# Optimization experiments

Hardware: AMD Instinct MI355X
Metric: run time of the kernel (lower is better)

The kernel has to match this reference:

```python
import jax, jax.numpy as jnp
import numpy as np

K = 8
DIM = 64
NUM_BLOCKS = 12
BN_EPS = 1e-5
LRELU_SLOPE = 0.01  # torch nn.LeakyReLU default negative_slope


def knn_indices(xyz, k):
    # xyz: [b, 3, n] -> idx [b, n, k] of k nearest neighbors (self included)
    x = jnp.transpose(xyz, (0, 2, 1))  # [b, n, 3]
    sq = jnp.sum(x * x, axis=-1)  # [b, n]
    d2 = sq[:, :, None] - 2.0 * jnp.einsum('bnd,bmd->bnm', x, x) + sq[:, None, :]
    _, idx = jax.lax.top_k(-d2, k)  # k smallest distances
    return idx


def group_point(points, idx):
    # points [b, d, n], idx [b, n, k] -> grouped [b, d, k, n]
    g = jax.vmap(lambda p, i: p[:, i])(points, idx)  # [b, d, n, k]
    return jnp.transpose(g, (0, 1, 3, 2))


def setup_inputs() -> dict:
    key = jax.random.key(0)
    ks = jax.random.split(key, 6)
    b, n = 8, 4096
    xyz = jax.random.normal(ks[0], (b, 3, n), dtype=jnp.float32)
    points = jax.random.normal(ks[1], (b, DIM, n), dtype=jnp.float32)
    # per-block params (note: the module's second Conv2d per block is never used
    # in forward — layers[4*idx+2] is applied to both center and grouped points)
    conv_w = jax.random.normal(ks[2], (NUM_BLOCKS, DIM, DIM), dtype=jnp.float32) * (1.0 / np.sqrt(DIM))
    conv_b = jax.random.normal(ks[3], (NUM_BLOCKS, DIM), dtype=jnp.float32) * 0.01
    bn_gamma = 1.0 + 0.1 * jax.random.normal(ks[4], (NUM_BLOCKS, DIM), dtype=jnp.float32)
    bn_beta = 0.1 * jax.random.normal(ks[5], (NUM_BLOCKS, DIM), dtype=jnp.float32)
    return {"xyz": xyz, "points": points, "conv_w": conv_w, "conv_b": conv_b,
            "bn_gamma": bn_gamma, "bn_beta": bn_beta}


def reference(xyz, points, conv_w, conv_b, bn_gamma, bn_beta):
    idx = knn_indices(xyz, K)  # fixed graph, computed once in block 0

    def block(p, params):
        w, b, g, be = params  # [DIM,DIM], [DIM], [DIM], [DIM]
        shortcut = p
        # BatchNorm1d (training-mode batch stats over batch & point dims)
        mean = jnp.mean(p, axis=(0, 2), keepdims=True)
        var = jnp.var(p, axis=(0, 2), keepdims=True)
        h = (p - mean) * jax.lax.rsqrt(var + BN_EPS) * g[None, :, None] + be[None, :, None]
        # LeakyReLU
        h = jnp.where(h >= 0, h, LRELU_SLOPE * h)
        # gather neighbor features: [b, d, k, n]
        grouped = group_point(h, idx)
        # shared 1x1 conv on center and grouped points
        center = jnp.einsum('od,bdn->bon', w, h) + b[None, :, None]            # [b,d,n]
        gconv = jnp.einsum('od,bdkn->bokn', w, grouped) + b[None, :, None, None]  # [b,d,k,n]
        # mean over concat([center[:, :, None], gconv], axis=2) == (center + sum_k gconv) / (k+1)
        new_p = (center + jnp.sum(gconv, axis=2)) / (K + 1) + shortcut
        return new_p, None

    out, _ = jax.lax.scan(block, points, (conv_w, conv_b, bn_gamma, bn_beta))
    return out
```

## Files before the change

kernel.cpp:

```cpp
#include <hip/hip_runtime.h>
#include <hip/hip_bf16.h>

#define NB     8
#define NPTS   4096
#define DIMC   64
#define KNN_K  8
#define NBLK   12
#define NREP   8

__global__ void zero_stats_kernel(float* __restrict__ stats) {
    int i = threadIdx.x + blockIdx.x * 256;
    if (i < 13 * NREP * 128) stats[i] = 0.0f;
}

__global__ __launch_bounds__(256) void prep_kernel(
        const float* __restrict__ xyz, float4* __restrict__ pts4g) {
#pragma clang fp contract(off)
    int g = blockIdx.x * 256 + threadIdx.x;
    int b = g >> 12, j = g & 4095;
    const float* xb = xyz + (size_t)b * 3 * NPTS;
    float x = xb[j];
    float y = xb[NPTS + j];
    float z = xb[2 * NPTS + j];
    float sq = (x * x + y * y) + z * z;
    pts4g[g] = make_float4(x, y, z, sq);
}

__global__ __launch_bounds__(256) void cast_kernel(
        const float* __restrict__ pts,
        float* __restrict__ P0, float* __restrict__ stats0) {
    __shared__ __align__(16) float tr[64 * 65];
    __shared__ float slotA[4 * 64], slotB[4 * 64];
    int wg = blockIdx.x;
    int b = wg & 7;
    int n0 = (wg >> 3) << 6;
    int rep = (wg >> 3) & (NREP - 1);
    int tid = threadIdx.x;
    int lane6 = tid & 63;
    int grp = tid >> 6;

    #pragma unroll
    for (int k = 0; k < 16; ++k) {
        int d = grp + (k << 2);
        float v = pts[(((size_t)((b << 6) + d)) << 12) + n0 + lane6];
        tr[d * 65 + lane6] = v;
    }
    __syncthreads();
    int c = lane6;
    float s = 0.0f, s2 = 0.0f;
    #pragma unroll
    for (int k = 0; k < 16; ++k) {
        int p = grp + (k << 2);
        float v = tr[c * 65 + p];
        P0[((size_t)((b << 12) + n0 + p)) * 64 + c] = v;
        s += v; s2 += v * v;
    }
    slotA[grp * 64 + c] = s;
    slotB[grp * 64 + c] = s2;
    __syncthreads();
    if (tid < 64) {
        float t = slotA[tid] + slotA[64 + tid] + slotA[128 + tid] + slotA[192 + tid];
        atomicAdd(&stats0[rep * 128 + tid], t);
    } else if (tid < 128) {
        int cc = tid - 64;
        float t = slotB[cc] + slotB[64 + cc] + slotB[128 + cc] + slotB[192 + cc];
        atomicAdd(&stats0[rep * 128 + 64 + cc], t);
    }
}

__global__ __launch_bounds__(512) void knn_kernel(
        const float4* __restrict__ pts4g, int* __restrict__ idx) {
#pragma clang fp contract(off)
    __shared__ __align__(16) float4 cand[2048];
    __shared__ double stash[4 * 9 * 128];
    int wg = blockIdx.x;
    int b = wg >> 5;
    int q0 = (wg & 31) << 7;
    int tid = threadIdx.x;

    int lane  = tid & 63;
    int wave  = tid >> 6;
    int chunk = wave & 3;
    int qgrp  = wave >> 2;
    int q_l   = (qgrp << 6) | lane;

    const float4* cb = pts4g + ((size_t)b << 12);
    float4 qp = cb[q0 + q_l];

    double k0, k1, k2, k3, k4, k5, k6, k7;
    k0 = k1 = k2 = k3 = k4 = k5 = k6 = k7 = __builtin_inf();
    float bd7f = 3.4e38f;

    for (int half = 0; half < 2; ++half) {
        if (half) __syncthreads();
        #pragma unroll
        for (int k = 0; k < 4; ++k)
            cand[tid + (k << 9)] = cb[(half << 11) + tid + (k << 9)];
        __syncthreads();

        int jl0 = chunk << 9;
        int jg0 = (half << 11) | (chunk << 9);
        int jstart = 0;

        if (half == 0) {
            for (int jo = 0; jo < 128; jo += 8) {
                float d2v[8];
                #pragma unroll
                for (int u = 0; u < 8; ++u) {
                    float4 p = cand[jl0 + jo + u];
                    float dot = (qp.x * p.x + qp.y * p.y) + qp.z * p.z;
                    d2v[u] = (qp.w - 2.0f * dot) + p.w;
                }
                #pragma unroll
                for (int u = 0; u < 8; ++u) {
                    unsigned long long kb =
                        __double_as_longlong((double)d2v[u]) |
                        (unsigned long long)(jg0 + jo + u);
                    double key = __longlong_as_double(kb);
                    double n0 = fmin(k0, key);
                    double n1 = fmin(k1, fmax(k0, key));
                    double n2 = fmin(k2, fmax(k1, key));
                    double n3 = fmin(k3, fmax(k2, key));
                    double n4 = fmin(k4, fmax(k3, key));
                    double n5 = fmin(k5, fmax(k4, key));
                    double n6 = fmin(k6, fmax(k5, key));
                    double n7 = fmin(k7, fmax(k6, key));
                    k0 = n0; k1 = n1; k2 = n2; k3 = n3;
                    k4 = n4; k5 = n5; k6 = n6; k7 = n7;
                }
            }
            bd7f = (float)k7;
            jstart = 128;
        }

        for (int jo = jstart; jo < 512; jo += 8) {
            float d2v[8];
            unsigned hm = 0u;
            #pragma unroll
            for (int u = 0; u < 8; ++u) {
                float4 p = cand[jl0 + jo + u];
                float dot = (qp.x * p.x + qp.y * p.y) + qp.z * p.z;
                float d2 = (qp.w - 2.0f * dot) + p.w;
                d2v[u] = d2;
                hm |= (d2 < bd7f) ? (1u << u) : 0u;
            }
            while (__any(hm != 0u)) {
                if (hm) {
                    int u = __builtin_ctz(hm);
                    hm &= hm - 1u;
                    float t0 = (u & 1) ? d2v[1] : d2v[0];
                    float t1 = (u & 1) ? d2v[3] : d2v[2];
                    float t2 = (u & 1) ? d2v[5] : d2v[4];
                    float t3 = (u & 1) ? d2v[7] : d2v[6];
                    float s0 = (u & 2) ? t1 : t0;
                    float s1 = (u & 2) ? t3 : t2;
                    float d2 = (u & 4) ? s1 : s0;
                    unsigned long long kb =
                        __double_as_longlong((double)d2) |
                        (unsigned long long)(jg0 + jo + u);
                    double key = __longlong_as_double(kb);
                    double n0 = fmin(k0, key);
                    double n1 = fmin(k1, fmax(k0, key));
                    double n2 = fmin(k2, fmax(k1, key));
                    double n3 = fmin(k3, fmax(k2, key));
                    double n4 = fmin(k4, fmax(k3, key));
                    double n5 = fmin(k5, fmax(k4, key));
                    double n6 = fmin(k6, fmax(k5, key));
                    double n7 = fmin(k7, fmax(k6, key));
                    k0 = n0; k1 = n1; k2 = n2; k3 = n3;
                    k4 = n4; k5 = n5; k6 = n6; k7 = n7;
                }
            }
            bd7f = (float)k7;
        }
    }

    {
        double* S = &stash[(chunk * 9) * 128 + q_l];
        S[0 * 128] = k0; S[1 * 128] = k1; S[2 * 128] = k2; S[3 * 128] = k3;
        S[4 * 128] = k4; S[5 * 128] = k5; S[6 * 128] = k6; S[7 * 128] = k7;
        S[8 * 128] = __builtin_inf();
    }
    __syncthreads();

    if (tid < 128) {
        int h0 = 0, h1 = 0, h2 = 0, h3 = 0;
        int* op = idx + ((size_t)(b * NPTS + q0 + tid)) * 8;
        #pragma unroll
        for (int t = 0; t < 8; ++t) {
            double b0 = stash[(0 * 9 + h0) * 128 + tid];
            double b1 = stash[(1 * 9 + h1) * 128 + tid];
            double b2 = stash[(2 * 9 + h2) * 128 + tid];
            double b3 = stash[(3 * 9 + h3) * 128 + tid];
            double best = b0; int bc = 0;
            if (b1 < best) { best = b1; bc = 1; }
            if (b2 < best) { best = b2; bc = 2; }
            if (b3 < best) { best = b3; bc = 3; }
            h0 += (bc == 0); h1 += (bc == 1);
            h2 += (bc == 2); h3 += (bc == 3);
            op[t] = (int)(__double_as_longlong(best) & 0xFFFULL);
        }
    }
}

__global__ __launch_bounds__(256) void block_kernel(
        const float* __restrict__ Pin, float* __restrict__ Pout,
        const float* __restrict__ statsIn, float* __restrict__ statsOut,
        const float* __restrict__ Wp, const float* __restrict__ Bp,
        const float* __restrict__ Gp, const float* __restrict__ Betap,
        const int* __restrict__ gidx, float* __restrict__ dout, int last) {
    __shared__ __align__(16) float Wt[64 * 68];
    __shared__ __align__(16) float mt[64 * 68];
    __shared__ __align__(16) float selft[64 * 64];
    __shared__ __align__(16) int   idxl[64 * 8];
    __shared__ __align__(16) float scale_l[64], shift_l[64], bias_l[64];
    __shared__ float slot[4 * 128];

    int wg = blockIdx.x;
    int b = wg & 7;
    int n0 = (wg >> 3) << 6;
    int rep = (wg >> 3) & (NREP - 1);
    int tid = threadIdx.x;

    const float* Pb = Pin + (((size_t)b) << 18);

    if (tid < 128) {
        ((int4*)idxl)[tid] = ((const int4*)(gidx + ((size_t)(b * NPTS + n0)) * 8))[tid];
    }
    #pragma unroll
    for (int k = 0; k < 4; ++k) {
        int lin = tid + (k << 8);
        ((float4*)selft)[lin] = ((const float4*)&Pb[(size_t)n0 << 6])[lin];
    }
    #pragma unroll
    for (int k = 0; k < 16; ++k) {
        int lin = tid + (k << 8);
        int o = lin >> 6, d = lin & 63;
        Wt[d * 68 + o] = Wp[lin];
    }
    if (tid < 64) {
        int c = tid;
        float sum = 0.0f, sumsq = 0.0f;
        #pragma unroll
        for (int r = 0; r < NREP; ++r) {
            sum   += statsIn[r * 128 + c];
            sumsq += statsIn[r * 128 + 64 + c];
        }
        float mean = sum * (1.0f / 32768.0f);
        float var  = sumsq * (1.0f / 32768.0f) - mean * mean;
        float rs   = 1.0f / sqrtf(var + 1e-5f);
        float sc   = Gp[c] * rs;
        scale_l[c] = sc;
        shift_l[c] = Betap[c] - mean * sc;
        bias_l[c]  = Bp[c];
    }
    __syncthreads();

    {
        int cq = tid & 15;
        int pg = tid >> 4;
        int c4 = cq << 2;
        float4 sc4 = *(const float4*)&scale_l[c4];
        float4 sh4 = *(const float4*)&shift_l[c4];
        #pragma unroll
        for (int i = 0; i < 4; ++i) {
            int pt = (pg << 2) + i;
            int4 ja = *(const int4*)&idxl[pt * 8];
            int4 jb = *(const int4*)&idxl[pt * 8 + 4];
            float4 v[9];
            v[0] = *(const float4*)&selft[(pt << 6) + c4];
            v[1] = *(const float4*)&Pb[(((size_t)ja.x) << 6) + c4];
            v[2] = *(const float4*)&Pb[(((size_t)ja.y) << 6) + c4];
            v[3] = *(const float4*)&Pb[(((size_t)ja.z) << 6) + c4];
            v[4] = *(const float4*)&Pb[(((size_t)ja.w) << 6) + c4];
            v[5] = *(const float4*)&Pb[(((size_t)jb.x) << 6) + c4];
            v[6] = *(const float4*)&Pb[(((size_t)jb.y) << 6) + c4];
            v[7] = *(const float4*)&Pb[(((size_t)jb.z) << 6) + c4];
            v[8] = *(const float4*)&Pb[(((size_t)jb.w) << 6) + c4];
            float4 a = make_float4(0.f, 0.f, 0.f, 0.f);
            #pragma unroll
            for (int k = 0; k < 9; ++k) {
                float hx = v[k].x * sc4.x + sh4.x;
                float hy = v[k].y * sc4.y + sh4.y;
                float hz = v[k].z * sc4.z + sh4.z;
                float hw = v[k].w * sc4.w + sh4.w;
                a.x += fmaxf(hx, 0.01f * hx);
                a.y += fmaxf(hy, 0.01f * hy);
                a.z += fmaxf(hz, 0.01f * hz);
                a.w += fmaxf(hw, 0.01f * hw);
            }
            mt[(c4 + 0) * 68 + pt] = a.x * (1.0f / 9.0f);
            mt[(c4 + 1) * 68 + pt] = a.y * (1.0f / 9.0f);
            mt[(c4 + 2) * 68 + pt] = a.z * (1.0f / 9.0f);
            mt[(c4 + 3) * 68 + pt] = a.w * (1.0f / 9.0f);
        }
    }
    __syncthreads();

    int o0 = (tid & 15) << 2;
    int p0 = (tid >> 4) << 2;
    float4 acc[4];
    {
        float4 bias4 = *(const float4*)&bias_l[o0];
        acc[0] = bias4; acc[1] = bias4; acc[2] = bias4; acc[3] = bias4;
    }
    #pragma unroll
    for (int d = 0; d < 64; ++d) {
        float4 wv = *(const float4*)&Wt[d * 68 + o0];
        float4 a  = *(const float4*)&mt[d * 68 + p0];
        acc[0].x += wv.x * a.x; acc[0].y += wv.y * a.x; acc[0].z += wv.z * a.x; acc[0].w += wv.w * a.x;
        acc[1].x += wv.x * a.y; acc[1].y += wv.y * a.y; acc[1].z += wv.z * a.y; acc[1].w += wv.w * a.y;
        acc[2].x += wv.x * a.z; acc[2].y += wv.y * a.z; acc[2].z += wv.z * a.z; acc[2].w += wv.w * a.z;
        acc[3].x += wv.x * a.w; acc[3].y += wv.y * a.w; acc[3].z += wv.z * a.w; acc[3].w += wv.w * a.w;
    }

    #pragma unroll
    for (int j = 0; j < 4; ++j) {
        float4 r = *(const float4*)&selft[((p0 + j) << 6) + o0];
        acc[j].x += r.x; acc[j].y += r.y; acc[j].z += r.z; acc[j].w += r.w;
    }

    if (!last) {
        float* PbOut = Pout + ((((size_t)b) << 12) + n0) * 64;
        #pragma unroll
        for (int j = 0; j < 4; ++j)
            *(float4*)&PbOut[((size_t)(p0 + j)) * 64 + o0] = acc[j];

        float4 s, s2;
        s.x = acc[0].x + acc[1].x + acc[2].x + acc[3].x;
        s.y = acc[0].y + acc[1].y + acc[2].y + acc[3].y;
        s.z = acc[0].z + acc[1].z + acc[2].z + acc[3].z;
        s.w = acc[0].w + acc[1].w + acc[2].w + acc[3].w;
        s2.x = acc[0].x*acc[0].x + acc[1].x*acc[1].x + acc[2].x*acc[2].x + acc[3].x*acc[3].x;
        s2.y = acc[0].y*acc[0].y + acc[1].y*acc[1].y + acc[2].y*acc[2].y + acc[3].y*acc[3].y;
        s2.z = acc[0].z*acc[0].z + acc[1].z*acc[1].z + acc[2].z*acc[2].z + acc[3].z*acc[3].z;
        s2.w = acc[0].w*acc[0].w + acc[1].w*acc[1].w + acc[2].w*acc[2].w + acc[3].w*acc[3].w;
        #pragma unroll
        for (int m = 16; m <= 32; m <<= 1) {
            s.x += __shfl_xor(s.x, m, 64);  s.y += __shfl_xor(s.y, m, 64);
            s.z += __shfl_xor(s.z, m, 64);  s.w += __shfl_xor(s.w, m, 64);
            s2.x += __shfl_xor(s2.x, m, 64); s2.y += __shfl_xor(s2.y, m, 64);
            s2.z += __shfl_xor(s2.z, m, 64); s2.w += __shfl_xor(s2.w, m, 64);
        }
        if ((tid & 63) < 16) {
            int w = tid >> 6;
            slot[w * 128 + o0 + 0] = s.x;  slot[w * 128 + o0 + 1] = s.y;
            slot[w * 128 + o0 + 2] = s.z;  slot[w * 128 + o0 + 3] = s.w;
            slot[w * 128 + 64 + o0 + 0] = s2.x; slot[w * 128 + 64 + o0 + 1] = s2.y;
            slot[w * 128 + 64 + o0 + 2] = s2.z; slot[w * 128 + 64 + o0 + 3] = s2.w;
        }
        __syncthreads();
        if (tid < 128) {
            float t = slot[tid] + slot[128 + tid] + slot[256 + tid] + slot[384 + tid];
            atomicAdd(&statsOut[rep * 128 + tid], t);
        }
    } else {
        __syncthreads();
        float* stage = mt;
        #pragma unroll
        for (int j = 0; j < 4; ++j) {
            stage[(o0 + 0) * 64 + p0 + j] = acc[j].x;
            stage[(o0 + 1) * 64 + p0 + j] = acc[j].y;
            stage[(o0 + 2) * 64 + p0 + j] = acc[j].z;
            stage[(o0 + 3) * 64 + p0 + j] = acc[j].w;
        }
        __syncthreads();
        #pragma unroll
        for (int k = 0; k < 16; ++k) {
            int lin = tid + (k << 8);
            int o = lin >> 6, pt = lin & 63;
            dout[(((size_t)((b << 6) + o)) << 12) + n0 + pt] = stage[lin];
        }
    }
}

extern "C" void kernel_launch(void* const* d_in, const int* in_sizes, int n_in,
                              void* d_out, int out_size, void* d_ws, size_t ws_size,
                              hipStream_t stream) {
    const float* xyz    = (const float*)d_in[0];
    const float* pts    = (const float*)d_in[1];
    const float* conv_w = (const float*)d_in[2];
    const float* conv_b = (const float*)d_in[3];
    const float* gamma  = (const float*)d_in[4];
    const float* beta   = (const float*)d_in[5];
    float* out = (float*)d_out;

    char* ws = (char*)d_ws;
    float*  P0    = (float*)(ws);
    float*  P1    = (float*)(ws + (size_t)8 * 1024 * 1024);
    int*    idx   = (int*)  (ws + (size_t)16 * 1024 * 1024);
    float*  stats = (float*)(ws + (size_t)17 * 1024 * 1024);
    float4* pts4g = (float4*)(ws + (size_t)18 * 1024 * 1024);

    zero_stats_kernel<<<52, 256, 0, stream>>>(stats);
    prep_kernel<<<128, 256, 0, stream>>>(xyz, pts4g);
    cast_kernel<<<512, 256, 0, stream>>>(pts, P0, stats);
    knn_kernel<<<256, 512, 0, stream>>>(pts4g, idx);

    float* Pbuf[2] = {P0, P1};
    for (int t = 0; t < NBLK; ++t) {
        block_kernel<<<512, 256, 0, stream>>>(
            Pbuf[t & 1], Pbuf[(t + 1) & 1],
            stats + (size_t)t * NREP * 128, stats + (size_t)(t + 1) * NREP * 128,
            conv_w + (size_t)t * 4096, conv_b + (size_t)t * 64,
            gamma + (size_t)t * 64, beta + (size_t)t * 64,
            idx, out, (t == NBLK - 1) ? 1 : 0);
    }
}
```

Measured before the change: 310.1 us.

## Split KNN candidate scan across 8 waves per 64 queries, double grid

Each workgroup of the KNN kernel now handles 64 queries instead of 128, with all 8 waves working on the same queries, each scanning a 256-candidate chunk per half. The final merge combines 8 sorted partial lists instead of 4, and the grid doubles to 512 workgroups with batch-interleaved mapping. This aims to raise parallelism and occupancy for the KNN search across the GPU's compute units. The cost is twice as many candidate loads into shared memory per query, a shorter warm-up before threshold pruning starts, and a longer merge step.

```diff
diff --git a/kernel.cpp b/kernel.cpp
--- a/kernel.cpp
+++ b/kernel.cpp
@@ -72,20 +72,17 @@
         const float4* __restrict__ pts4g, int* __restrict__ idx) {
 #pragma clang fp contract(off)
     __shared__ __align__(16) float4 cand[2048];
-    __shared__ double stash[4 * 9 * 128];
+    __shared__ double stash[8 * 9 * 64];
     int wg = blockIdx.x;
-    int b = wg >> 5;
-    int q0 = (wg & 31) << 7;
+    int b = wg & 7;
+    int q0 = (wg >> 3) << 6;
     int tid = threadIdx.x;
 
     int lane  = tid & 63;
-    int wave  = tid >> 6;
-    int chunk = wave & 3;
-    int qgrp  = wave >> 2;
-    int q_l   = (qgrp << 6) | lane;
+    int chunk = tid >> 6;
 
     const float4* cb = pts4g + ((size_t)b << 12);
-    float4 qp = cb[q0 + q_l];
+    float4 qp = cb[q0 + lane];
 
     double k0, k1, k2, k3, k4, k5, k6, k7;
     k0 = k1 = k2 = k3 = k4 = k5 = k6 = k7 = __builtin_inf();
@@ -98,12 +95,12 @@
             cand[tid + (k << 9)] = cb[(half << 11) + tid + (k << 9)];
         __syncthreads();
 
-        int jl0 = chunk << 9;
-        int jg0 = (half << 11) | (chunk << 9);
+        int jl0 = chunk << 8;
+        int jg0 = (half << 11) | (chunk << 8);
         int jstart = 0;
 
         if (half == 0) {
-            for (int jo = 0; jo < 128; jo += 8) {
+            for (int jo = 0; jo < 32; jo += 8) {
                 float d2v[8];
                 #pragma unroll
                 for (int u = 0; u < 8; ++u) {
@@ -130,10 +127,10 @@
                 }
             }
             bd7f = (float)k7;
-            jstart = 128;
-        }
-
-        for (int jo = jstart; jo < 512; jo += 8) {
+            jstart = 32;
+        }
+
+        for (int jo = jstart; jo < 256; jo += 8) {
             float d2v[8];
             unsigned hm = 0u;
             #pragma unroll
@@ -176,28 +173,38 @@
     }
 
     {
-        double* S = &stash[(chunk * 9) * 128 + q_l];
-        S[0 * 128] = k0; S[1 * 128] = k1; S[2 * 128] = k2; S[3 * 128] = k3;
-        S[4 * 128] = k4; S[5 * 128] = k5; S[6 * 128] = k6; S[7 * 128] = k7;
-        S[8 * 128] = __builtin_inf();
+        double* S = &stash[(chunk * 9) * 64 + lane];
+        S[0 * 64] = k0; S[1 * 64] = k1; S[2 * 64] = k2; S[3 * 64] = k3;
+        S[4 * 64] = k4; S[5 * 64] = k5; S[6 * 64] = k6; S[7 * 64] = k7;
+        S[8 * 64] = __builtin_inf();
     }
     __syncthreads();
 
-    if (tid < 128) {
-        int h0 = 0, h1 = 0, h2 = 0, h3 = 0;
+    if (tid < 64) {
+        int h0 = 0, h1 = 0, h2 = 0, h3 = 0, h4 = 0, h5 = 0, h6 = 0, h7 = 0;
         int* op = idx + ((size_t)(b * NPTS + q0 + tid)) * 8;
         #pragma unroll
         for (int t = 0; t < 8; ++t) {
-            double b0 = stash[(0 * 9 + h0) * 128 + tid];
-            double b1 = stash[(1 * 9 + h1) * 128 + tid];
-            double b2 = stash[(2 * 9 + h2) * 128 + tid];
-            double b3 = stash[(3 * 9 + h3) * 128 + tid];
-            double best = b0; int bc = 0;
-            if (b1 < best) { best = b1; bc = 1; }
-            if (b2 < best) { best = b2; bc = 2; }
-            if (b3 < best) { best = b3; bc = 3; }
+            double c0 = stash[(0 * 9 + h0) * 64 + tid];
+            double c1 = stash[(1 * 9 + h1) * 64 + tid];
+            double c2 = stash[(2 * 9 + h2) * 64 + tid];
+            double c3 = stash[(3 * 9 + h3) * 64 + tid];
+            double c4 = stash[(4 * 9 + h4) * 64 + tid];
+            double c5 = stash[(5 * 9 + h5) * 64 + tid];
+            double c6 = stash[(6 * 9 + h6) * 64 + tid];
+            double c7 = stash[(7 * 9 + h7) * 64 + tid];
+            double best = c0; int bc = 0;
+            if (c1 < best) { best = c1; bc = 1; }
+            if (c2 < best) { best = c2; bc = 2; }
+            if (c3 < best) { best = c3; bc = 3; }
+            if (c4 < best) { best = c4; bc = 4; }
+            if (c5 < best) { best = c5; bc = 5; }
+            if (c6 < best) { best = c6; bc = 6; }
+            if (c7 < best) { best = c7; bc = 7; }
             h0 += (bc == 0); h1 += (bc == 1);
             h2 += (bc == 2); h3 += (bc == 3);
+            h4 += (bc == 4); h5 += (bc == 5);
+            h6 += (bc == 6); h7 += (bc == 7);
             op[t] = (int)(__double_as_longlong(best) & 0xFFFULL);
         }
     }
@@ -395,7 +402,7 @@
     zero_stats_kernel<<<52, 256, 0, stream>>>(stats);
     prep_kernel<<<128, 256, 0, stream>>>(xyz, pts4g);
     cast_kernel<<<512, 256, 0, stream>>>(pts, P0, stats);
-    knn_kernel<<<256, 512, 0, stream>>>(pts4g, idx);
+    knn_kernel<<<512, 512, 0, stream>>>(pts4g, idx);
 
     float* Pbuf[2] = {P0, P1};
     for (int t = 0; t < NBLK; ++t) {
```

Measured after the change: 313.2 us. Within noise of the previous version (+1.0%).

## Fuse twelve block launches into one persistent kernel with grid barriers

Applied to the files above, without the earlier changes.

The twelve per-block launches are replaced by a single persistent kernel that loops over blocks and uses an atomic-counter grid barrier between them, removing per-launch overhead and idle gaps. The stats zeroing is folded into the prep kernel, which also clears the barrier counters. The kNN kernel drops its LDS candidate staging and instead streams candidates directly from global memory with register double-buffering, each wave scanning a 1024-point chunk. The grid barrier assumes all 512 workgroups are co-resident, otherwise it deadlocks. Each block also reloads the weights and its tile every iteration.

```diff
diff --git a/kernel.cpp b/kernel.cpp
--- a/kernel.cpp
+++ b/kernel.cpp
@@ -7,16 +7,15 @@
 #define KNN_K  8
 #define NBLK   12
 #define NREP   8
-
-__global__ void zero_stats_kernel(float* __restrict__ stats) {
-    int i = threadIdx.x + blockIdx.x * 256;
-    if (i < 13 * NREP * 128) stats[i] = 0.0f;
-}
+#define NWG    512
 
 __global__ __launch_bounds__(256) void prep_kernel(
-        const float* __restrict__ xyz, float4* __restrict__ pts4g) {
+        const float* __restrict__ xyz, float4* __restrict__ pts4g,
+        float* __restrict__ stats, int* __restrict__ bar) {
 #pragma clang fp contract(off)
     int g = blockIdx.x * 256 + threadIdx.x;
+    if (g < 13 * NREP * 128) stats[g] = 0.0f;
+    if (g < 16) bar[g] = 0;
     int b = g >> 12, j = g & 4095;
     const float* xb = xyz + (size_t)b * 3 * NPTS;
     float x = xb[j];
@@ -68,10 +67,22 @@
     }
 }
 
+#define INS(KEY) do { \
+    double key = (KEY); \
+    double n0 = fmin(k0, key); \
+    double n1 = fmin(k1, fmax(k0, key)); \
+    double n2 = fmin(k2, fmax(k1, key)); \
+    double n3 = fmin(k3, fmax(k2, key)); \
+    double n4 = fmin(k4, fmax(k3, key)); \
+    double n5 = fmin(k5, fmax(k4, key)); \
+    double n6 = fmin(k6, fmax(k5, key)); \
+    double n7 = fmin(k7, fmax(k6, key)); \
+    k0 = n0; k1 = n1; k2 = n2; k3 = n3; \
+    k4 = n4; k5 = n5; k6 = n6; k7 = n7; } while (0)
+
 __global__ __launch_bounds__(512) void knn_kernel(
         const float4* __restrict__ pts4g, int* __restrict__ idx) {
 #pragma clang fp contract(off)
-    __shared__ __align__(16) float4 cand[2048];
     __shared__ double stash[4 * 9 * 128];
     int wg = blockIdx.x;
     int b = wg >> 5;
@@ -91,87 +102,72 @@
     k0 = k1 = k2 = k3 = k4 = k5 = k6 = k7 = __builtin_inf();
     float bd7f = 3.4e38f;
 
-    for (int half = 0; half < 2; ++half) {
-        if (half) __syncthreads();
-        #pragma unroll
-        for (int k = 0; k < 4; ++k)
-            cand[tid + (k << 9)] = cb[(half << 11) + tid + (k << 9)];
-        __syncthreads();
-
-        int jl0 = chunk << 9;
-        int jg0 = (half << 11) | (chunk << 9);
-        int jstart = 0;
-
-        if (half == 0) {
-            for (int jo = 0; jo < 128; jo += 8) {
-                float d2v[8];
-                #pragma unroll
-                for (int u = 0; u < 8; ++u) {
-                    float4 p = cand[jl0 + jo + u];
-                    float dot = (qp.x * p.x + qp.y * p.y) + qp.z * p.z;
-                    d2v[u] = (qp.w - 2.0f * dot) + p.w;
-                }
-                #pragma unroll
-                for (int u = 0; u < 8; ++u) {
-                    unsigned long long kb =
-                        __double_as_longlong((double)d2v[u]) |
-                        (unsigned long long)(jg0 + jo + u);
-                    double key = __longlong_as_double(kb);
-                    double n0 = fmin(k0, key);
-                    double n1 = fmin(k1, fmax(k0, key));
-                    double n2 = fmin(k2, fmax(k1, key));
-                    double n3 = fmin(k3, fmax(k2, key));
-                    double n4 = fmin(k4, fmax(k3, key));
-                    double n5 = fmin(k5, fmax(k4, key));
-                    double n6 = fmin(k6, fmax(k5, key));
-                    double n7 = fmin(k7, fmax(k6, key));
-                    k0 = n0; k1 = n1; k2 = n2; k3 = n3;
-                    k4 = n4; k5 = n5; k6 = n6; k7 = n7;
-                }
-            }
-            bd7f = (float)k7;
-            jstart = 128;
-        }
-
-        for (int jo = jstart; jo < 512; jo += 8) {
-            float d2v[8];
-            unsigned hm = 0u;
-            #pragma unroll
-            for (int u = 0; u < 8; ++u) {
-                float4 p = cand[jl0 + jo + u];
-                float dot = (qp.x * p.x + qp.y * p.y) + qp.z * p.z;
-                float d2 = (qp.w - 2.0f * dot) + p.w;
-                d2v[u] = d2;
-                hm |= (d2 < bd7f) ? (1u << u) : 0u;
-            }
-            while (__any(hm != 0u)) {
-                if (hm) {
-                    int u = __builtin_ctz(hm);
-                    hm &= hm - 1u;
-                    float t0 = (u & 1) ? d2v[1] : d2v[0];
-                    float t1 = (u & 1) ? d2v[3] : d2v[2];
-                    float t2 = (u & 1) ? d2v[5] : d2v[4];
-                    float t3 = (u & 1) ? d2v[7] : d2v[6];
-                    float s0 = (u & 2) ? t1 : t0;
-                    float s1 = (u & 2) ? t3 : t2;
-                    float d2 = (u & 4) ? s1 : s0;
-                    unsigned long long kb =
-                        __double_as_longlong((double)d2) |
-                        (unsigned long long)(jg0 + jo + u);
-                    double key = __longlong_as_double(kb);
-                    double n0 = fmin(k0, key);
-                    double n1 = fmin(k1, fmax(k0, key));
-                    double n2 = fmin(k2, fmax(k1, key));
-                    double n3 = fmin(k3, fmax(k2, key));
-                    double n4 = fmin(k4, fmax(k3, key));
-                    double n5 = fmin(k5, fmax(k4, key));
-                    double n6 = fmin(k6, fmax(k5, key));
-                    double n7 = fmin(k7, fmax(k6, key));
-                    k0 = n0; k1 = n1; k2 = n2; k3 = n3;
-                    k4 = n4; k5 = n5; k6 = n6; k7 = n7;
-                }
-            }
-            bd7f = (float)k7;
+    int chu = __builtin_amdgcn_readfirstlane(chunk);
+    const float4* cc = cb + ((size_t)chu << 10);
+    int jg0 = chu << 10;
+
+    float4 pc[8];
+    #pragma unroll
+    for (int u = 0; u < 8; ++u) pc[u] = cc[u];
+
+    for (int jo = 0; jo < 128; jo += 8) {
+        float4 pn[8];
+        #pragma unroll
+        for (int u = 0; u < 8; ++u) pn[u] = cc[jo + 8 + u];
+        float d2v[8];
+        #pragma unroll
+        for (int u = 0; u < 8; ++u) {
+            float dot = (qp.x * pc[u].x + qp.y * pc[u].y) + qp.z * pc[u].z;
+            d2v[u] = (qp.w - 2.0f * dot) + pc[u].w;
+        }
+        #pragma unroll
+        for (int u = 0; u < 8; ++u) {
+            unsigned long long kb =
+                __double_as_longlong((double)d2v[u]) |
+                (unsigned long long)(jg0 + jo + u);
+            INS(__longlong_as_double(kb));
+        }
+        #pragma unroll
+        for (int u = 0; u < 8; ++u) pc[u] = pn[u];
+    }
+    bd7f = (float)k7;
+
+    for (int jo = 128; jo < 1024; jo += 8) {
+        float4 pn[8];
+        if (jo + 8 < 1024) {
+            #pragma unroll
+            for (int u = 0; u < 8; ++u) pn[u] = cc[jo + 8 + u];
+        }
+        float d2v[8];
+        unsigned hm = 0u;
+        #pragma unroll
+        for (int u = 0; u < 8; ++u) {
+            float dot = (qp.x * pc[u].x + qp.y * pc[u].y) + qp.z * pc[u].z;
+            float d2 = (qp.w - 2.0f * dot) + pc[u].w;
+            d2v[u] = d2;
+            hm |= (d2 < bd7f) ? (1u << u) : 0u;
+        }
+        while (__any(hm != 0u)) {
+            if (hm) {
+                int u = __builtin_ctz(hm);
+                hm &= hm - 1u;
+                float t0 = (u & 1) ? d2v[1] : d2v[0];
+                float t1 = (u & 1) ? d2v[3] : d2v[2];
+                float t2 = (u & 1) ? d2v[5] : d2v[4];
+                float t3 = (u & 1) ? d2v[7] : d2v[6];
+                float s0 = (u & 2) ? t1 : t0;
+                float s1 = (u & 2) ? t3 : t2;
+                float d2 = (u & 4) ? s1 : s0;
+                unsigned long long kb =
+                    __double_as_longlong((double)d2) |
+                    (unsigned long long)(jg0 + jo + u);
+                INS(__longlong_as_double(kb));
+            }
+        }
+        bd7f = (float)k7;
+        if (jo + 8 < 1024) {
+            #pragma unroll
+            for (int u = 0; u < 8; ++u) pc[u] = pn[u];
         }
     }
 
@@ -203,12 +199,13 @@
     }
 }
 
-__global__ __launch_bounds__(256) void block_kernel(
-        const float* __restrict__ Pin, float* __restrict__ Pout,
-        const float* __restrict__ statsIn, float* __restrict__ statsOut,
-        const float* __restrict__ Wp, const float* __restrict__ Bp,
-        const float* __restrict__ Gp, const float* __restrict__ Betap,
-        const int* __restrict__ gidx, float* __restrict__ dout, int last) {
+__global__ __launch_bounds__(256) void blocks_kernel(
+        float* __restrict__ P0, float* __restrict__ P1,
+        float* __restrict__ stats,
+        const float* __restrict__ conv_w, const float* __restrict__ conv_b,
+        const float* __restrict__ gamma, const float* __restrict__ beta,
+        const int* __restrict__ gidx, float* __restrict__ dout,
+        int* __restrict__ bar) {
     __shared__ __align__(16) float Wt[64 * 68];
     __shared__ __align__(16) float mt[64 * 68];
     __shared__ __align__(16) float selft[64 * 64];
@@ -222,154 +219,181 @@
     int rep = (wg >> 3) & (NREP - 1);
     int tid = threadIdx.x;
 
-    const float* Pb = Pin + (((size_t)b) << 18);
-
     if (tid < 128) {
         ((int4*)idxl)[tid] = ((const int4*)(gidx + ((size_t)(b * NPTS + n0)) * 8))[tid];
     }
-    #pragma unroll
-    for (int k = 0; k < 4; ++k) {
-        int lin = tid + (k << 8);
-        ((float4*)selft)[lin] = ((const float4*)&Pb[(size_t)n0 << 6])[lin];
-    }
-    #pragma unroll
-    for (int k = 0; k < 16; ++k) {
-        int lin = tid + (k << 8);
-        int o = lin >> 6, d = lin & 63;
-        Wt[d * 68 + o] = Wp[lin];
-    }
-    if (tid < 64) {
-        int c = tid;
-        float sum = 0.0f, sumsq = 0.0f;
-        #pragma unroll
-        for (int r = 0; r < NREP; ++r) {
-            sum   += statsIn[r * 128 + c];
-            sumsq += statsIn[r * 128 + 64 + c];
-        }
-        float mean = sum * (1.0f / 32768.0f);
-        float var  = sumsq * (1.0f / 32768.0f) - mean * mean;
-        float rs   = 1.0f / sqrtf(var + 1e-5f);
-        float sc   = Gp[c] * rs;
-        scale_l[c] = sc;
-        shift_l[c] = Betap[c] - mean * sc;
-        bias_l[c]  = Bp[c];
-    }
-    __syncthreads();
-
-    {
-        int cq = tid & 15;
-        int pg = tid >> 4;
-        int c4 = cq << 2;
-        float4 sc4 = *(const float4*)&scale_l[c4];
-        float4 sh4 = *(const float4*)&shift_l[c4];
-        #pragma unroll
-        for (int i = 0; i < 4; ++i) {
-            int pt = (pg << 2) + i;
-            int4 ja = *(const int4*)&idxl[pt * 8];
-            int4 jb = *(const int4*)&idxl[pt * 8 + 4];
-            float4 v[9];
-            v[0] = *(const float4*)&selft[(pt << 6) + c4];
-            v[1] = *(const float4*)&Pb[(((size_t)ja.x) << 6) + c4];
-            v[2] = *(const float4*)&Pb[(((size_t)ja.y) << 6) + c4];
-            v[3] = *(const float4*)&Pb[(((size_t)ja.z) << 6) + c4];
-            v[4] = *(const float4*)&Pb[(((size_t)ja.w) << 6) + c4];
-            v[5] = *(const float4*)&Pb[(((size_t)jb.x) << 6) + c4];
-            v[6] = *(const float4*)&Pb[(((size_t)jb.y) << 6) + c4];
-            v[7] = *(const float4*)&Pb[(((size_t)jb.z) << 6) + c4];
-            v[8] = *(const float4*)&Pb[(((size_t)jb.w) << 6) + c4];
-            float4 a = make_float4(0.f, 0.f, 0.f, 0.f);
-            #pragma unroll
-            for (int k = 0; k < 9; ++k) {
-                float hx = v[k].x * sc4.x + sh4.x;
-                float hy = v[k].y * sc4.y + sh4.y;
-                float hz = v[k].z * sc4.z + sh4.z;
-                float hw = v[k].w * sc4.w + sh4.w;
-                a.x += fmaxf(hx, 0.01f * hx);
-                a.y += fmaxf(hy, 0.01f * hy);
-                a.z += fmaxf(hz, 0.01f * hz);
-                a.w += fmaxf(hw, 0.01f * hw);
-            }
-            mt[(c4 + 0) * 68 + pt] = a.x * (1.0f / 9.0f);
-            mt[(c4 + 1) * 68 + pt] = a.y * (1.0f / 9.0f);
-            mt[(c4 + 2) * 68 + pt] = a.z * (1.0f / 9.0f);
-            mt[(c4 + 3) * 68 + pt] = a.w * (1.0f / 9.0f);
-        }
-    }
-    __syncthreads();
-
-    int o0 = (tid & 15) << 2;
-    int p0 = (tid >> 4) << 2;
-    float4 acc[4];
-    {
-        float4 bias4 = *(const float4*)&bias_l[o0];
-        acc[0] = bias4; acc[1] = bias4; acc[2] = bias4; acc[3] = bias4;
-    }
-    #pragma unroll
-    for (int d = 0; d < 64; ++d) {
-        float4 wv = *(const float4*)&Wt[d * 68 + o0];
-        float4 a  = *(const float4*)&mt[d * 68 + p0];
-        acc[0].x += wv.x * a.x; acc[0].y += wv.y * a.x; acc[0].z += wv.z * a.x; acc[0].w += wv.w * a.x;
-        acc[1].x += wv.x * a.y; acc[1].y += wv.y * a.y; acc[1].z += wv.z * a.y; acc[1].w += wv.w * a.y;
-        acc[2].x += wv.x * a.z; acc[2].y += wv.y * a.z; acc[2].z += wv.z * a.z; acc[2].w += wv.w * a.z;
-        acc[3].x += wv.x * a.w; acc[3].y += wv.y * a.w; acc[3].z += wv.z * a.w; acc[3].w += wv.w * a.w;
-    }
-
-    #pragma unroll
-    for (int j = 0; j < 4; ++j) {
-        float4 r = *(const float4*)&selft[((p0 + j) << 6) + o0];
-        acc[j].x += r.x; acc[j].y += r.y; acc[j].z += r.z; acc[j].w += r.w;
-    }
-
-    if (!last) {
-        float* PbOut = Pout + ((((size_t)b) << 12) + n0) * 64;
-        #pragma unroll
-        for (int j = 0; j < 4; ++j)
-            *(float4*)&PbOut[((size_t)(p0 + j)) * 64 + o0] = acc[j];
-
-        float4 s, s2;
-        s.x = acc[0].x + acc[1].x + acc[2].x + acc[3].x;
-        s.y = acc[0].y + acc[1].y + acc[2].y + acc[3].y;
-        s.z = acc[0].z + acc[1].z + acc[2].z + acc[3].z;
-        s.w = acc[0].w + acc[1].w + acc[2].w + acc[3].w;
-        s2.x = acc[0].x*acc[0].x + acc[1].x*acc[1].x + acc[2].x*acc[2].x + acc[3].x*acc[3].x;
-        s2.y = acc[0].y*acc[0].y + acc[1].y*acc[1].y + acc[2].y*acc[2].y + acc[3].y*acc[3].y;
-        s2.z = acc[0].z*acc[0].z + acc[1].z*acc[1].z + acc[2].z*acc[2].z + acc[3].z*acc[3].z;
-        s2.w = acc[0].w*acc[0].w + acc[1].w*acc[1].w + acc[2].w*acc[2].w + acc[3].w*acc[3].w;
-        #pragma unroll
-        for (int m = 16; m <= 32; m <<= 1) {
-            s.x += __shfl_xor(s.x, m, 64);  s.y += __shfl_xor(s.y, m, 64);
-            s.z += __shfl_xor(s.z, m, 64);  s.w += __shfl_xor(s.w, m, 64);
-            s2.x += __shfl_xor(s2.x, m, 64); s2.y += __shfl_xor(s2.y, m, 64);
-            s2.z += __shfl_xor(s2.z, m, 64); s2.w += __shfl_xor(s2.w, m, 64);
-        }
-        if ((tid & 63) < 16) {
-            int w = tid >> 6;
-            slot[w * 128 + o0 + 0] = s.x;  slot[w * 128 + o0 + 1] = s.y;
-            slot[w * 128 + o0 + 2] = s.z;  slot[w * 128 + o0 + 3] = s.w;
-            slot[w * 128 + 64 + o0 + 0] = s2.x; slot[w * 128 + 64 + o0 + 1] = s2.y;
-            slot[w * 128 + 64 + o0 + 2] = s2.z; slot[w * 128 + 64 + o0 + 3] = s2.w;
-        }
-        __syncthreads();
-        if (tid < 128) {
-            float t = slot[tid] + slot[128 + tid] + slot[256 + tid] + slot[384 + tid];
-            atomicAdd(&statsOut[rep * 128 + tid], t);
-        }
-    } else {
-        __syncthreads();
-        float* stage = mt;
-        #pragma unroll
-        for (int j = 0; j < 4; ++j) {
-            stage[(o0 + 0) * 64 + p0 + j] = acc[j].x;
-            stage[(o0 + 1) * 64 + p0 + j] = acc[j].y;
-            stage[(o0 + 2) * 64 + p0 + j] = acc[j].z;
-            stage[(o0 + 3) * 64 + p0 + j] = acc[j].w;
-        }
-        __syncthreads();
+
+    for (int t = 0; t < NBLK; ++t) {
+        const float* Pin  = (t & 1) ? P1 : P0;
+        float*       Pout = (t & 1) ? P0 : P1;
+        const float* statsIn  = stats + (size_t)t * NREP * 128;
+        float*       statsOut = stats + (size_t)(t + 1) * NREP * 128;
+        const float* Wp    = conv_w + (size_t)t * 4096;
+        const float* Bp    = conv_b + (size_t)t * 64;
+        const float* Gp    = gamma  + (size_t)t * 64;
+        const float* Betap = beta   + (size_t)t * 64;
+        int last = (t == NBLK - 1);
+
+        const float* Pb = Pin + (((size_t)b) << 18);
+
+        #pragma unroll
+        for (int k = 0; k < 4; ++k) {
+            int lin = tid + (k << 8);
+            ((float4*)selft)[lin] = ((const float4*)&Pb[(size_t)n0 << 6])[lin];
+        }
         #pragma unroll
         for (int k = 0; k < 16; ++k) {
             int lin = tid + (k << 8);
-            int o = lin >> 6, pt = lin & 63;
-            dout[(((size_t)((b << 6) + o)) << 12) + n0 + pt] = stage[lin];
+            int o = lin >> 6, d = lin & 63;
+            Wt[d * 68 + o] = Wp[lin];
+        }
+        if (tid < 64) {
+            int c = tid;
+            float sum = 0.0f, sumsq = 0.0f;
+            #pragma unroll
+            for (int r = 0; r < NREP; ++r) {
+                sum   += statsIn[r * 128 + c];
+                sumsq += statsIn[r * 128 + 64 + c];
+            }
+            float mean = sum * (1.0f / 32768.0f);
+            float var  = sumsq * (1.0f / 32768.0f) - mean * mean;
+            float rs   = 1.0f / sqrtf(var + 1e-5f);
+            float sc   = Gp[c] * rs;
+            scale_l[c] = sc;
+            shift_l[c] = Betap[c] - mean * sc;
+            bias_l[c]  = Bp[c];
+        }
+        __syncthreads();
+
+        {
+            int cq = tid & 15;
+            int pg = tid >> 4;
+            int c4 = cq << 2;
+            float4 sc4 = *(const float4*)&scale_l[c4];
+            float4 sh4 = *(const float4*)&shift_l[c4];
+            #pragma unroll
+            for (int i = 0; i < 4; ++i) {
+                int pt = (pg << 2) + i;
+                int4 ja = *(const int4*)&idxl[pt * 8];
+                int4 jb = *(const int4*)&idxl[pt * 8 + 4];
+                float4 v[9];
+                v[0] = *(const float4*)&selft[(pt << 6) + c4];
+                v[1] = *(const float4*)&Pb[(((size_t)ja.x) << 6) + c4];
+                v[2] = *(const float4*)&Pb[(((size_t)ja.y) << 6) + c4];
+                v[3] = *(const float4*)&Pb[(((size_t)ja.z) << 6) + c4];
+                v[4] = *(const float4*)&Pb[(((size_t)ja.w) << 6) + c4];
+                v[5] = *(const float4*)&Pb[(((size_t)jb.x) << 6) + c4];
+                v[6] = *(const float4*)&Pb[(((size_t)jb.y) << 6) + c4];
+                v[7] = *(const float4*)&Pb[(((size_t)jb.z) << 6) + c4];
+                v[8] = *(const float4*)&Pb[(((size_t)jb.w) << 6) + c4];
+                float4 a = make_float4(0.f, 0.f, 0.f, 0.f);
+                #pragma unroll
+                for (int k = 0; k < 9; ++k) {
+                    float hx = v[k].x * sc4.x + sh4.x;
+                    float hy = v[k].y * sc4.y + sh4.y;
+                    float hz = v[k].z * sc4.z + sh4.z;
+                    float hw = v[k].w * sc4.w + sh4.w;
+                    a.x += fmaxf(hx, 0.01f * hx);
+                    a.y += fmaxf(hy, 0.01f * hy);
+                    a.z += fmaxf(hz, 0.01f * hz);
+                    a.w += fmaxf(hw, 0.01f * hw);
+                }
+                mt[(c4 + 0) * 68 + pt] = a.x * (1.0f / 9.0f);
+                mt[(c4 + 1) * 68 + pt] = a.y * (1.0f / 9.0f);
+                mt[(c4 + 2) * 68 + pt] = a.z * (1.0f / 9.0f);
+                mt[(c4 + 3) * 68 + pt] = a.w * (1.0f / 9.0f);
+            }
+        }
+        __syncthreads();
+
+        int o0 = (tid & 15) << 2;
+        int p0 = (tid >> 4) << 2;
+        float4 acc[4];
+        {
+            float4 bias4 = *(const float4*)&bias_l[o0];
+            acc[0] = bias4; acc[1] = bias4; acc[2] = bias4; acc[3] = bias4;
+        }
+        #pragma unroll
+        for (int d = 0; d < 64; ++d) {
+            float4 wv = *(const float4*)&Wt[d * 68 + o0];
+            float4 a  = *(const float4*)&mt[d * 68 + p0];
+            acc[0].x += wv.x * a.x; acc[0].y += wv.y * a.x; acc[0].z += wv.z * a.x; acc[0].w += wv.w * a.x;
+            acc[1].x += wv.x * a.y; acc[1].y += wv.y * a.y; acc[1].z += wv.z * a.y; acc[1].w += wv.w * a.y;
+            acc[2].x += wv.x * a.z; acc[2].y += wv.y * a.z; acc[2].z += wv.z * a.z; acc[2].w += wv.w * a.z;
+            acc[3].x += wv.x * a.w; acc[3].y += wv.y * a.w; acc[3].z += wv.z * a.w; acc[3].w += wv.w * a.w;
+        }
+
+        #pragma unroll
+        for (int j = 0; j < 4; ++j) {
+            float4 r = *(const float4*)&selft[((p0 + j) << 6) + o0];
+            acc[j].x += r.x; acc[j].y += r.y; acc[j].z += r.z; acc[j].w += r.w;
+        }
+
+        if (!last) {
+            float* PbOut = Pout + ((((size_t)b) << 12) + n0) * 64;
+            #pragma unroll
+            for (int j = 0; j < 4; ++j)
+                *(float4*)&PbOut[((size_t)(p0 + j)) * 64 + o0] = acc[j];
+
+            float4 s, s2;
+            s.x = acc[0].x + acc[1].x + acc[2].x + acc[3].x;
+            s.y = acc[0].y + acc[1].y + acc[2].y + acc[3].y;
+            s.z = acc[0].z + acc[1].z + acc[2].z + acc[3].z;
+            s.w = acc[0].w + acc[1].w + acc[2].w + acc[3].w;
+            s2.x = acc[0].x*acc[0].x + acc[1].x*acc[1].x + acc[2].x*acc[2].x + acc[3].x*acc[3].x;
+            s2.y = acc[0].y*acc[0].y + acc[1].y*acc[1].y + acc[2].y*acc[2].y + acc[3].y*acc[3].y;
+            s2.z = acc[0].z*acc[0].z + acc[1].z*acc[1].z + acc[2].z*acc[2].z + acc[3].z*acc[3].z;
+            s2.w = acc[0].w*acc[0].w + acc[1].w*acc[1].w + acc[2].w*acc[2].w + acc[3].w*acc[3].w;
+            #pragma unroll
+            for (int m = 16; m <= 32; m <<= 1) {
+                s.x += __shfl_xor(s.x, m, 64);  s.y += __shfl_xor(s.y, m, 64);
+                s.z += __shfl_xor(s.z, m, 64);  s.w += __shfl_xor(s.w, m, 64);
+                s2.x += __shfl_xor(s2.x, m, 64); s2.y += __shfl_xor(s2.y, m, 64);
+                s2.z += __shfl_xor(s2.z, m, 64); s2.w += __shfl_xor(s2.w, m, 64);
+            }
+            if ((tid & 63) < 16) {
+                int w = tid >> 6;
+                slot[w * 128 + o0 + 0] = s.x;  slot[w * 128 + o0 + 1] = s.y;
+                slot[w * 128 + o0 + 2] = s.z;  slot[w * 128 + o0 + 3] = s.w;
+                slot[w * 128 + 64 + o0 + 0] = s2.x; slot[w * 128 + 64 + o0 + 1] = s2.y;
+                slot[w * 128 + 64 + o0 + 2] = s2.z; slot[w * 128 + 64 + o0 + 3] = s2.w;
+            }
+            __syncthreads();
+            if (tid < 128) {
+                float tt = slot[tid] + slot[128 + tid] + slot[256 + tid] + slot[384 + tid];
+                atomicAdd(&statsOut[rep * 128 + tid], tt);
+            }
+
+            __syncthreads();
+            if (tid == 0) {
+                __threadfence();
+                int a = __hip_atomic_fetch_add(&bar[t], 1,
+                            __ATOMIC_ACQ_REL, __HIP_MEMORY_SCOPE_AGENT);
+                if (a + 1 < NWG) {
+                    while (__hip_atomic_load(&bar[t],
+                                __ATOMIC_ACQUIRE, __HIP_MEMORY_SCOPE_AGENT) < NWG)
+                        __builtin_amdgcn_s_sleep(1);
+                }
+                __threadfence();
+            }
+            __syncthreads();
+        } else {
+            __syncthreads();
+            float* stage = mt;
+            #pragma unroll
+            for (int j = 0; j < 4; ++j) {
+                stage[(o0 + 0) * 64 + p0 + j] = acc[j].x;
+                stage[(o0 + 1) * 64 + p0 + j] = acc[j].y;
+                stage[(o0 + 2) * 64 + p0 + j] = acc[j].z;
+                stage[(o0 + 3) * 64 + p0 + j] = acc[j].w;
+            }
+            __syncthreads();
+            #pragma unroll
+            for (int k = 0; k < 16; ++k) {
+                int lin = tid + (k << 8);
+                int o = lin >> 6, pt = lin & 63;
+                dout[(((size_t)((b << 6) + o)) << 12) + n0 + pt] = stage[lin];
+            }
         }
     }
 }
@@ -390,20 +414,13 @@
     float*  P1    = (float*)(ws + (size_t)8 * 1024 * 1024);
     int*    idx   = (int*)  (ws + (size_t)16 * 1024 * 1024);
     float*  stats = (float*)(ws + (size_t)17 * 1024 * 1024);
+    int*    bar   = (int*)  (ws + (size_t)17 * 1024 * 1024 + 64 * 1024);
     float4* pts4g = (float4*)(ws + (size_t)18 * 1024 * 1024);
 
-    zero_stats_kernel<<<52, 256, 0, stream>>>(stats);
-    prep_kernel<<<128, 256, 0, stream>>>(xyz, pts4g);
+    prep_kernel<<<128, 256, 0, stream>>>(xyz, pts4g, stats, bar);
     cast_kernel<<<512, 256, 0, stream>>>(pts, P0, stats);
     knn_kernel<<<256, 512, 0, stream>>>(pts4g, idx);
 
-    float* Pbuf[2] = {P0, P1};
-    for (int t = 0; t < NBLK; ++t) {
-        block_kernel<<<512, 256, 0, stream>>>(
-            Pbuf[t & 1], Pbuf[(t + 1) & 1],
-            stats + (size_t)t * NREP * 128, stats + (size_t)(t + 1) * NREP * 128,
-            conv_w + (size_t)t * 4096, conv_b + (size_t)t * 64,
-            gamma + (size_t)t * 64, beta + (size_t)t * 64,
-            idx, out, (t == NBLK - 1) ? 1 : 0);
-    }
+    blocks_kernel<<<NWG, 256, 0, stream>>>(
+        P0, P1, stats, conv_w, conv_b, gamma, beta, idx, out, bar);
 }
```

Result: slower. 843.6 us (+172.1%).
